# Optimization experiments

Measured on AMD Instinct MI355X. Metric: run time of the kernel, lower is better.

## Reference

```python
import jax, jax.numpy as jnp
import numpy as np

MODEL_DIM = 1024
NUM_HEADS = 16
HEAD_DIM = MODEL_DIM // NUM_HEADS


def setup_inputs() -> dict:
    key = jax.random.key(0)
    ks = jax.random.split(key, 5)
    B, T, D = 4, 2048, MODEL_DIM
    scale = 1.0 / np.sqrt(D)
    x = jax.random.normal(ks[0], (B, T, D), dtype=jnp.float32)
    W_qkv = jax.random.normal(ks[1], (D, 3 * D), dtype=jnp.float32) * scale
    b_qkv = jnp.zeros((3 * D,), dtype=jnp.float32)
    W_out = jax.random.normal(ks[2], (D, D), dtype=jnp.float32) * scale
    b_out = jnp.zeros((D,), dtype=jnp.float32)
    return {"x": x, "W_qkv": W_qkv, "b_qkv": b_qkv, "W_out": W_out, "b_out": b_out}


def reference(x, W_qkv, b_qkv, W_out, b_out):
    B, T, D = x.shape
    H, Hd = NUM_HEADS, HEAD_DIM
    qkv = x @ W_qkv + b_qkv                      # [B,T,3D]
    q, k, v = jnp.split(qkv, 3, axis=-1)
    # [B,T,D] -> [B,H,T,Hd]
    q = q.reshape(B, T, H, Hd).transpose(0, 2, 1, 3)
    k = k.reshape(B, T, H, Hd).transpose(0, 2, 1, 3)
    v = v.reshape(B, T, H, Hd).transpose(0, 2, 1, 3)
    scores = jnp.einsum('bhqd,bhkd->bhqk', q, k) * (1.0 / np.sqrt(Hd))
    causal = jnp.tril(jnp.ones((T, T), dtype=bool))
    scores = jnp.where(causal[None, None], scores, -jnp.inf)
    attn = jax.nn.softmax(scores, axis=-1)
    out = jnp.einsum('bhqk,bhkd->bhqd', attn, v)  # [B,H,T,Hd]
    out = out.transpose(0, 2, 1, 3).reshape(B, T, D)
    return out @ W_out + b_out
```

## Files before the change

### kernel.cpp

```cpp
#include <hip/hip_runtime.h>
#include <stdint.h>

#define T_SEQ   2048
#define DMODEL  1024
#define NHEADS  16
#define HDIM    64
#define BATCH   4
#define MROWS   (BATCH * T_SEQ)
#define QSCALE  0.18033688011112042f
#define DEFER_THR 6.0f

typedef __attribute__((ext_vector_type(4))) short bf16x4;
typedef __attribute__((ext_vector_type(8))) short bf16x8;
typedef __attribute__((ext_vector_type(4))) float f32x4;

__device__ __forceinline__ unsigned short f2b(float f) {
    union { float f; unsigned int i; } x;
    x.f = f;
    unsigned int r = x.i + 0x7FFFu + ((x.i >> 16) & 1u);
    return (unsigned short)(r >> 16);
}

__device__ __forceinline__ float fexp2(float x) {
#if __has_builtin(__builtin_amdgcn_exp2f)
    return __builtin_amdgcn_exp2f(x);
#else
    return __expf(x * 0.6931471805599453f);
#endif
}

__device__ __forceinline__ unsigned int pack2(float a, float b) {
#if __has_builtin(__builtin_amdgcn_cvt_pk_bf16_f32)
    auto r = __builtin_amdgcn_cvt_pk_bf16_f32(a, b);
    unsigned int u;
    __builtin_memcpy(&u, &r, 4);
    return u;
#else
    return ((unsigned int)f2b(a)) | (((unsigned int)f2b(b)) << 16);
#endif
}

__device__ __forceinline__ float max16(const f32x4 s[4]) {
    const float a = fmaxf(fmaxf(s[0][0], s[0][1]), fmaxf(s[0][2], s[0][3]));
    const float b = fmaxf(fmaxf(s[1][0], s[1][1]), fmaxf(s[1][2], s[1][3]));
    const float c = fmaxf(fmaxf(s[2][0], s[2][1]), fmaxf(s[2][2], s[2][3]));
    const float d = fmaxf(fmaxf(s[3][0], s[3][1]), fmaxf(s[3][2], s[3][3]));
    return fmaxf(fmaxf(a, b), fmaxf(c, d));
}

__device__ __forceinline__ void online_softmax(
    const f32x4 sg[4], float& m_, float& l_, f32x4 o_[4], bf16x4 pf_[4])
{
    float mc = max16(sg);
    mc = fmaxf(mc, __shfl_xor(mc, 16));
    mc = fmaxf(mc, __shfl_xor(mc, 32));
    if (__any(mc > m_ + DEFER_THR)) {
        const float mn    = fmaxf(m_, mc);
        const float alpha = fexp2(m_ - mn);
        l_ *= alpha;
        #pragma unroll
        for (int dt = 0; dt < 4; dt++)
            #pragma unroll
            for (int r = 0; r < 4; r++) o_[dt][r] *= alpha;
        m_ = mn;
    }
    float ps = 0.f;
    #pragma unroll
    for (int s = 0; s < 4; s++) {
        const float p0 = fexp2(sg[s][0] - m_);
        const float p1 = fexp2(sg[s][1] - m_);
        const float p2 = fexp2(sg[s][2] - m_);
        const float p3 = fexp2(sg[s][3] - m_);
        ps += (p0 + p1) + (p2 + p3);
        uint2 u;
        u.x = pack2(p0, p1);
        u.y = pack2(p2, p3);
        pf_[s] = *(bf16x4*)&u;
    }
    ps += __shfl_xor(ps, 16);
    ps += __shfl_xor(ps, 32);
    l_ += ps;
}

__device__ __forceinline__ void gl_lds16(const unsigned short* g, unsigned short* l) {
    __builtin_amdgcn_global_load_lds(
        (const __attribute__((address_space(1))) void*)g,
        (__attribute__((address_space(3))) void*)l,
        16, 0, 0);
}

__global__ __launch_bounds__(256) void cvt_bf16(
    const float* __restrict__ in, unsigned short* __restrict__ out, int n)
{
    const int i = (blockIdx.x * 256 + threadIdx.x) * 4;
    if (i + 3 < n) {
        const float4 v = *(const float4*)(in + i);
        ushort4 o;
        o.x = f2b(v.x); o.y = f2b(v.y); o.z = f2b(v.z); o.w = f2b(v.w);
        *(ushort4*)(out + i) = o;
    }
}

__global__ __launch_bounds__(256) void cvt_tr(
    const float* __restrict__ W, unsigned short* __restrict__ WT, int K, int N)
{
    __shared__ unsigned short s[32][33];
    const int n0 = blockIdx.x * 32, k0 = blockIdx.y * 32;
    const int tx = threadIdx.x & 31, ty = threadIdx.x >> 5;
    #pragma unroll
    for (int i = 0; i < 4; i++)
        s[ty + 8 * i][tx] = f2b(W[(size_t)(k0 + ty + 8 * i) * N + n0 + tx]);
    __syncthreads();
    #pragma unroll
    for (int i = 0; i < 4; i++)
        WT[(size_t)(n0 + ty + 8 * i) * K + k0 + tx] = s[tx][ty + 8 * i];
}

template<int KD, int NCOLS, int MODE>
__global__ __launch_bounds__(256) void gemm_mfma(
    const unsigned short* __restrict__ A,
    const unsigned short* __restrict__ BT,
    const float* __restrict__ bias,
    unsigned short* __restrict__ Oq,
    unsigned short* __restrict__ Ok,
    unsigned short* __restrict__ Ov,
    float* __restrict__ Of)
{
    __shared__ __align__(16) unsigned short aS[128 * 64];
    __shared__ __align__(16) unsigned short bS[128 * 64];

    const int tid  = threadIdx.x;
    const int lane = tid & 63;
    const int wave = tid >> 6;
    const int row  = lane & 15;
    const int quad = lane >> 4;
    const int wm   = wave >> 1;
    const int wn   = wave & 1;
    const int m0   = blockIdx.y * 128;
    const int n0   = blockIdx.x * 128;

    const int srow = lane >> 3;
    const int c8   = lane & 7;
    const int csw  = c8 ^ srow;

    const unsigned short* aG = A  + (size_t)(m0 + wave * 8 + srow) * KD + csw * 8;
    const unsigned short* bG = BT + (size_t)(n0 + wave * 8 + srow) * KD + csw * 8;

    f32x4 acc[4][4];
    const f32x4 z = {0.f, 0.f, 0.f, 0.f};
    #pragma unroll
    for (int i = 0; i < 4; i++)
        #pragma unroll
        for (int j = 0; j < 4; j++) acc[i][j] = z;

    for (int k0 = 0; k0 < KD; k0 += 64) {
        __syncthreads();
        #pragma unroll
        for (int c = 0; c < 4; c++) {
            gl_lds16(aG + c * (32 * KD), &aS[c * 2048 + wave * 512]);
            gl_lds16(bG + c * (32 * KD), &bS[c * 2048 + wave * 512]);
        }
        __syncthreads();
        aG += 64;
        bG += 64;

        #pragma unroll
        for (int ks = 0; ks < 2; ks++) {
            bf16x8 af[4], bf[4];
            const int cp = ((ks * 4 + quad) ^ (row & 7)) * 8;
            #pragma unroll
            for (int t = 0; t < 4; t++) {
                af[t] = *(const bf16x8*)(aS + (wm * 64 + t * 16 + row) * 64 + cp);
                bf[t] = *(const bf16x8*)(bS + (wn * 64 + t * 16 + row) * 64 + cp);
            }
            #pragma unroll
            for (int i = 0; i < 4; i++)
                #pragma unroll
                for (int j = 0; j < 4; j++)
                    acc[i][j] = __builtin_amdgcn_mfma_f32_16x16x32_bf16(af[i], bf[j], acc[i][j], 0, 0, 0);
        }
    }

    if (MODE == 0) {
        #pragma unroll
        for (int j = 0; j < 4; j++) {
            const int n  = n0 + wn * 64 + j * 16 + row;
            const float bi = bias[n];
            const int which = n >> 10;
            const int rem   = n & 1023;
            const int h     = rem >> 6;
            const int d     = rem & 63;
            #pragma unroll
            for (int i = 0; i < 4; i++) {
                const int mbase = m0 + wm * 64 + i * 16 + quad * 4;
                #pragma unroll
                for (int r = 0; r < 4; r++) {
                    const int m = mbase + r;
                    const int b = m >> 11;
                    const int t = m & 2047;
                    const int bh = b * NHEADS + h;
                    const float v = acc[i][j][r] + bi;
                    if (which == 0) {
                        Oq[((size_t)bh * T_SEQ + t) * HDIM + d] = f2b(v * QSCALE);
                    } else if (which == 1) {
                        Ok[((size_t)bh * T_SEQ + t) * HDIM + d] = f2b(v);
                    } else {
                        Ov[((size_t)bh * HDIM + d) * T_SEQ + t] = f2b(v);
                    }
                }
            }
        }
    } else {
        #pragma unroll
        for (int j = 0; j < 4; j++) {
            const int n  = n0 + wn * 64 + j * 16 + row;
            const float bi = bias[n];
            #pragma unroll
            for (int i = 0; i < 4; i++) {
                const int mbase = m0 + wm * 64 + i * 16 + quad * 4;
                #pragma unroll
                for (int r = 0; r < 4; r++)
                    Of[(size_t)(mbase + r) * NCOLS + n] = acc[i][j][r] + bi;
            }
        }
    }
}

__global__ __launch_bounds__(512, 4) void attn_mfma(
    const unsigned short* __restrict__ Q,
    const unsigned short* __restrict__ K,
    const unsigned short* __restrict__ VT,
    unsigned short* __restrict__ Out)
{
    __shared__ __align__(16) unsigned short kS[2][64 * 72];
    __shared__ __align__(16) unsigned short vS[2][64 * 72];

    const int tid  = threadIdx.x;
    const int lane = tid & 63;
    const int wave = tid >> 6;
    const int row  = lane & 15;
    const int quad = lane >> 4;

    const int bh = blockIdx.x;
    const int b  = bh >> 4;
    const int h  = bh & 15;
    const int P  = blockIdx.y;
    const int q0H = 128 * (15 - P) + 16 * wave;
    const int q0L = 128 * P        + 16 * wave;
    const int kend = 128 * (15 - P) + 128;

    const size_t qkbase = (size_t)bh * T_SEQ * HDIM;
    const size_t vtbase = (size_t)bh * HDIM * T_SEQ;

    const int krow0 = tid >> 3;
    const int c0    = tid & 7;
    const int lds0  = krow0 * 72 + c0 * 8;
    const int flat0 = tid * 8;

    const unsigned short* qpH = Q + qkbase + (size_t)(q0H + row) * HDIM + quad * 8;
    const bf16x8 qH0 = *(const bf16x8*)qpH;
    const bf16x8 qH1 = *(const bf16x8*)(qpH + 32);
    const unsigned short* qpL = Q + qkbase + (size_t)(q0L + row) * HDIM + quad * 8;
    const bf16x8 qL0 = *(const bf16x8*)qpL;
    const bf16x8 qL1 = *(const bf16x8*)(qpL + 32);

    const f32x4 z = {0.f, 0.f, 0.f, 0.f};
    f32x4 oH[4] = {z, z, z, z};
    f32x4 oL[4] = {z, z, z, z};
    float mH = -1e30f, lH = 0.f, mL = -1e30f, lL = 0.f;

    uint4 pk0 = *(const uint4*)(K  + qkbase + flat0);
    uint4 pv0 = *(const uint4*)(VT + vtbase + (size_t)krow0 * T_SEQ + c0 * 8);

    int buf = 0;
    for (int kb = 0; kb < kend; kb += 64) {
        *(uint4*)&kS[buf][lds0] = pk0;
        *(uint4*)&vS[buf][lds0] = pv0;
        __syncthreads();

        if (kb + 64 < kend) {
            const int kn = kb + 64;
            pk0 = *(const uint4*)(K  + qkbase + (size_t)kn * HDIM + flat0);
            pv0 = *(const uint4*)(VT + vtbase + (size_t)krow0 * T_SEQ + kn + c0 * 8);
        }

        const bool actH = (kb <= q0H);
        const bool actL = (kb <= q0L);

        bf16x4 pfH[4], pfL[4];

        if (actH) {
            f32x4 sH[4], sL[4];
            #pragma unroll
            for (int s = 0; s < 4; s++) {
                const int kbs = kb + s * 16;
                if (kbs <= q0H) {
                    const unsigned short* kp = &kS[buf][(s * 16 + row) * 72 + quad * 8];
                    const bf16x8 kf0 = *(const bf16x8*)kp;
                    const bf16x8 kf1 = *(const bf16x8*)(kp + 32);
                    f32x4 t = z;
                    t = __builtin_amdgcn_mfma_f32_16x16x32_bf16(kf0, qH0, t, 0, 0, 0);
                    t = __builtin_amdgcn_mfma_f32_16x16x32_bf16(kf1, qH1, t, 0, 0, 0);
                    if (kbs == q0H) {
                        #pragma unroll
                        for (int r = 0; r < 4; r++)
                            if (quad * 4 + r > row) t[r] = -1e30f;
                    }
                    sH[s] = t;
                    if (kbs <= q0L) {
                        f32x4 u = z;
                        u = __builtin_amdgcn_mfma_f32_16x16x32_bf16(kf0, qL0, u, 0, 0, 0);
                        u = __builtin_amdgcn_mfma_f32_16x16x32_bf16(kf1, qL1, u, 0, 0, 0);
                        if (kbs == q0L) {
                            #pragma unroll
                            for (int r = 0; r < 4; r++)
                                if (quad * 4 + r > row) u[r] = -1e30f;
                        }
                        sL[s] = u;
                    } else {
                        #pragma unroll
                        for (int r = 0; r < 4; r++) sL[s][r] = -1e30f;
                    }
                } else {
                    #pragma unroll
                    for (int r = 0; r < 4; r++) { sH[s][r] = -1e30f; sL[s][r] = -1e30f; }
                }
            }
            online_softmax(sH, mH, lH, oH, pfH);
            if (actL)
                online_softmax(sL, mL, lL, oL, pfL);

            #pragma unroll
            for (int s = 0; s < 4; s++) {
                const int kbs = kb + s * 16;
                if (kbs <= q0H) {
                    #pragma unroll
                    for (int dt = 0; dt < 4; dt++) {
                        const bf16x4 vf = *(const bf16x4*)&vS[buf][
                            (dt * 16 + row) * 72 + (s * 2 + (quad >> 1)) * 8 + (quad & 1) * 4];
                        oH[dt] = __builtin_amdgcn_mfma_f32_16x16x16bf16_1k(vf, pfH[s], oH[dt], 0, 0, 0);
                        if (kbs <= q0L)
                            oL[dt] = __builtin_amdgcn_mfma_f32_16x16x16bf16_1k(vf, pfL[s], oL[dt], 0, 0, 0);
                    }
                }
            }
        }

        buf ^= 1;
    }

    {
        const float rl = 1.f / lH;
        unsigned short* op = Out + ((size_t)(b * T_SEQ + q0H + row)) * DMODEL + h * HDIM + quad * 4;
        #pragma unroll
        for (int dt = 0; dt < 4; dt++) {
            uint2 u;
            u.x = pack2(oH[dt][0] * rl, oH[dt][1] * rl);
            u.y = pack2(oH[dt][2] * rl, oH[dt][3] * rl);
            *(uint2*)(op + dt * 16) = u;
        }
    }
    {
        const float rl = 1.f / lL;
        unsigned short* op = Out + ((size_t)(b * T_SEQ + q0L + row)) * DMODEL + h * HDIM + quad * 4;
        #pragma unroll
        for (int dt = 0; dt < 4; dt++) {
            uint2 u;
            u.x = pack2(oL[dt][0] * rl, oL[dt][1] * rl);
            u.y = pack2(oL[dt][2] * rl, oL[dt][3] * rl);
            *(uint2*)(op + dt * 16) = u;
        }
    }
}

extern "C" void kernel_launch(void* const* d_in, const int* in_sizes, int n_in,
                              void* d_out, int out_size, void* d_ws, size_t ws_size,
                              hipStream_t stream)
{
    const float* x    = (const float*)d_in[0];
    const float* Wqkv = (const float*)d_in[1];
    const float* bqkv = (const float*)d_in[2];
    const float* Wout = (const float*)d_in[3];
    const float* bout = (const float*)d_in[4];
    float* out = (float*)d_out;

    char* ws = (char*)d_ws;
    unsigned short* xb    = (unsigned short*)(ws + (size_t)0  * 1024 * 1024);
    unsigned short* WqkvT = (unsigned short*)(ws + (size_t)16 * 1024 * 1024);
    unsigned short* WoutT = (unsigned short*)(ws + (size_t)22 * 1024 * 1024);
    unsigned short* Qb    = (unsigned short*)(ws + (size_t)24 * 1024 * 1024);
    unsigned short* Kb    = (unsigned short*)(ws + (size_t)40 * 1024 * 1024);
    unsigned short* Vt    = (unsigned short*)(ws + (size_t)56 * 1024 * 1024);
    unsigned short* Ab    = (unsigned short*)(ws + (size_t)72 * 1024 * 1024);

    cvt_bf16<<<dim3(MROWS * DMODEL / 1024), 256, 0, stream>>>(x, xb, MROWS * DMODEL);
    cvt_tr<<<dim3(3 * DMODEL / 32, DMODEL / 32), 256, 0, stream>>>(Wqkv, WqkvT, DMODEL, 3 * DMODEL);
    cvt_tr<<<dim3(DMODEL / 32, DMODEL / 32), 256, 0, stream>>>(Wout, WoutT, DMODEL, DMODEL);

    gemm_mfma<DMODEL, 3 * DMODEL, 0><<<dim3(3 * DMODEL / 128, MROWS / 128), 256, 0, stream>>>(
        xb, WqkvT, bqkv, Qb, Kb, Vt, nullptr);

    attn_mfma<<<dim3(BATCH * NHEADS, 8), 512, 0, stream>>>(Qb, Kb, Vt, Ab);

    gemm_mfma<DMODEL, DMODEL, 1><<<dim3(DMODEL / 128, MROWS / 128), 256, 0, stream>>>(
        Ab, WoutT, bout, nullptr, nullptr, nullptr, out);
}
```

Baseline: 293.7 us.

## Add 256x256-tile 8-wave QKV GEMM with double-buffered direct-to-LDS loads

```diff
diff --git a/kernel.cpp b/kernel.cpp
--- a/kernel.cpp
+++ b/kernel.cpp
@@ -116,14 +116,190 @@
         WT[(size_t)(n0 + ty + 8 * i) * K + k0 + tx] = s[tx][ty + 8 * i];
 }
 
-template<int KD, int NCOLS, int MODE>
-__global__ __launch_bounds__(256) void gemm_mfma(
+__global__ __launch_bounds__(512, 2) void gemm_qkv8(
     const unsigned short* __restrict__ A,
     const unsigned short* __restrict__ BT,
     const float* __restrict__ bias,
     unsigned short* __restrict__ Oq,
     unsigned short* __restrict__ Ok,
-    unsigned short* __restrict__ Ov,
+    unsigned short* __restrict__ Ov)
+{
+    constexpr int KD = DMODEL;
+    constexpr int NK = KD / 64;
+    __shared__ __align__(16) unsigned short aS[2 * 256 * 64];
+    __shared__ __align__(16) unsigned short bS[2 * 256 * 64];
+
+    const int tid   = threadIdx.x;
+    const int lane  = tid & 63;
+    const int wave  = tid >> 6;
+    const int row16 = lane & 15;
+    const int quadL = lane >> 4;
+    const int wm    = wave >> 2;
+    const int wn    = wave & 3;
+    const int n0    = blockIdx.x * 256;
+    const int m0    = blockIdx.y * 256;
+
+    const int lrow = lane >> 3;
+    const int csw  = (lane & 7) ^ lrow;
+
+    const unsigned short* aB = A  + (size_t)(m0 + wave * 8 + lrow) * KD + csw * 8;
+    const unsigned short* bB = BT + (size_t)(n0 + wave * 8 + lrow) * KD + csw * 8;
+    unsigned short* aD = &aS[wave * 512];
+    unsigned short* bD = &bS[wave * 512];
+
+    const int sw0 = (quadL)     ^ (row16 & 7);
+    const int sw1 = (4 + quadL) ^ (row16 & 7);
+    const int aO  = (wm * 128 + row16) * 64;
+    const int bO  = (wn * 64  + row16) * 64;
+
+    f32x4 acc[8][4];
+    const f32x4 z = {0.f, 0.f, 0.f, 0.f};
+    #pragma unroll
+    for (int i = 0; i < 8; i++)
+        #pragma unroll
+        for (int j = 0; j < 4; j++) acc[i][j] = z;
+
+    gl_lds16(aB,                      aD);
+    gl_lds16(aB + (size_t)64  * KD,   aD + 64  * 64);
+    gl_lds16(aB + (size_t)128 * KD,   aD + 128 * 64);
+    gl_lds16(aB + (size_t)192 * KD,   aD + 192 * 64);
+    gl_lds16(bB,                      bD);
+    gl_lds16(bB + (size_t)64  * KD,   bD + 64  * 64);
+    gl_lds16(bB + (size_t)128 * KD,   bD + 128 * 64);
+    gl_lds16(bB + (size_t)192 * KD,   bD + 192 * 64);
+
+    for (int j = 0; j < NK; ++j) {
+        const int rb   = (j & 1) * 16384;
+        const int wb   = rb ^ 16384;
+        const int ksrc = (j + 1 < NK) ? (j + 1) * 64 : 0;
+        const unsigned short* aPk = aB + ksrc;
+        const unsigned short* bPk = bB + ksrc;
+
+        bf16x8 bfr[4][2];
+        bf16x8 a0, a1, a2, a3;
+
+        gl_lds16(aPk,                    aD + wb);
+        gl_lds16(aPk + (size_t)64 * KD,  aD + wb + 64 * 64);
+        asm volatile("s_waitcnt vmcnt(2)" ::: "memory");
+        __builtin_amdgcn_s_barrier();
+        #pragma unroll
+        for (int nf = 0; nf < 4; ++nf) {
+            bfr[nf][0] = *(const bf16x8*)&bS[rb + bO + nf * 1024 + sw0 * 8];
+            bfr[nf][1] = *(const bf16x8*)&bS[rb + bO + nf * 1024 + sw1 * 8];
+        }
+        a0 = *(const bf16x8*)&aS[rb + aO + 0 * 1024 + sw0 * 8];
+        a1 = *(const bf16x8*)&aS[rb + aO + 0 * 1024 + sw1 * 8];
+        a2 = *(const bf16x8*)&aS[rb + aO + 1 * 1024 + sw0 * 8];
+        a3 = *(const bf16x8*)&aS[rb + aO + 1 * 1024 + sw1 * 8];
+        asm volatile("s_waitcnt lgkmcnt(0)" ::: "memory");
+        __builtin_amdgcn_sched_barrier(0);
+        __builtin_amdgcn_s_setprio(1);
+        #pragma unroll
+        for (int nf = 0; nf < 4; ++nf) {
+            acc[0][nf] = __builtin_amdgcn_mfma_f32_16x16x32_bf16(a0, bfr[nf][0], acc[0][nf], 0, 0, 0);
+            acc[0][nf] = __builtin_amdgcn_mfma_f32_16x16x32_bf16(a1, bfr[nf][1], acc[0][nf], 0, 0, 0);
+            acc[1][nf] = __builtin_amdgcn_mfma_f32_16x16x32_bf16(a2, bfr[nf][0], acc[1][nf], 0, 0, 0);
+            acc[1][nf] = __builtin_amdgcn_mfma_f32_16x16x32_bf16(a3, bfr[nf][1], acc[1][nf], 0, 0, 0);
+        }
+        __builtin_amdgcn_s_setprio(0);
+        __builtin_amdgcn_s_barrier();
+
+        gl_lds16(aPk + (size_t)128 * KD, aD + wb + 128 * 64);
+        gl_lds16(aPk + (size_t)192 * KD, aD + wb + 192 * 64);
+        a0 = *(const bf16x8*)&aS[rb + aO + 2 * 1024 + sw0 * 8];
+        a1 = *(const bf16x8*)&aS[rb + aO + 2 * 1024 + sw1 * 8];
+        a2 = *(const bf16x8*)&aS[rb + aO + 3 * 1024 + sw0 * 8];
+        a3 = *(const bf16x8*)&aS[rb + aO + 3 * 1024 + sw1 * 8];
+        __builtin_amdgcn_s_barrier();
+        asm volatile("s_waitcnt lgkmcnt(0)" ::: "memory");
+        __builtin_amdgcn_sched_barrier(0);
+        __builtin_amdgcn_s_setprio(1);
+        #pragma unroll
+        for (int nf = 0; nf < 4; ++nf) {
+            acc[2][nf] = __builtin_amdgcn_mfma_f32_16x16x32_bf16(a0, bfr[nf][0], acc[2][nf], 0, 0, 0);
+            acc[2][nf] = __builtin_amdgcn_mfma_f32_16x16x32_bf16(a1, bfr[nf][1], acc[2][nf], 0, 0, 0);
+            acc[3][nf] = __builtin_amdgcn_mfma_f32_16x16x32_bf16(a2, bfr[nf][0], acc[3][nf], 0, 0, 0);
+            acc[3][nf] = __builtin_amdgcn_mfma_f32_16x16x32_bf16(a3, bfr[nf][1], acc[3][nf], 0, 0, 0);
+        }
+        __builtin_amdgcn_s_setprio(0);
+        __builtin_amdgcn_s_barrier();
+
+        gl_lds16(bPk,                    bD + wb);
+        gl_lds16(bPk + (size_t)64 * KD,  bD + wb + 64 * 64);
+        a0 = *(const bf16x8*)&aS[rb + aO + 4 * 1024 + sw0 * 8];
+        a1 = *(const bf16x8*)&aS[rb + aO + 4 * 1024 + sw1 * 8];
+        a2 = *(const bf16x8*)&aS[rb + aO + 5 * 1024 + sw0 * 8];
+        a3 = *(const bf16x8*)&aS[rb + aO + 5 * 1024 + sw1 * 8];
+        __builtin_amdgcn_s_barrier();
+        asm volatile("s_waitcnt lgkmcnt(0)" ::: "memory");
+        __builtin_amdgcn_sched_barrier(0);
+        __builtin_amdgcn_s_setprio(1);
+        #pragma unroll
+        for (int nf = 0; nf < 4; ++nf) {
+            acc[4][nf] = __builtin_amdgcn_mfma_f32_16x16x32_bf16(a0, bfr[nf][0], acc[4][nf], 0, 0, 0);
+            acc[4][nf] = __builtin_amdgcn_mfma_f32_16x16x32_bf16(a1, bfr[nf][1], acc[4][nf], 0, 0, 0);
+            acc[5][nf] = __builtin_amdgcn_mfma_f32_16x16x32_bf16(a2, bfr[nf][0], acc[5][nf], 0, 0, 0);
+            acc[5][nf] = __builtin_amdgcn_mfma_f32_16x16x32_bf16(a3, bfr[nf][1], acc[5][nf], 0, 0, 0);
+        }
+        __builtin_amdgcn_s_setprio(0);
+        __builtin_amdgcn_s_barrier();
+
+        gl_lds16(bPk + (size_t)128 * KD, bD + wb + 128 * 64);
+        gl_lds16(bPk + (size_t)192 * KD, bD + wb + 192 * 64);
+        a0 = *(const bf16x8*)&aS[rb + aO + 6 * 1024 + sw0 * 8];
+        a1 = *(const bf16x8*)&aS[rb + aO + 6 * 1024 + sw1 * 8];
+        a2 = *(const bf16x8*)&aS[rb + aO + 7 * 1024 + sw0 * 8];
+        a3 = *(const bf16x8*)&aS[rb + aO + 7 * 1024 + sw1 * 8];
+        __builtin_amdgcn_s_barrier();
+        asm volatile("s_waitcnt lgkmcnt(0)" ::: "memory");
+        __builtin_amdgcn_sched_barrier(0);
+        __builtin_amdgcn_s_setprio(1);
+        #pragma unroll
+        for (int nf = 0; nf < 4; ++nf) {
+            acc[6][nf] = __builtin_amdgcn_mfma_f32_16x16x32_bf16(a0, bfr[nf][0], acc[6][nf], 0, 0, 0);
+            acc[6][nf] = __builtin_amdgcn_mfma_f32_16x16x32_bf16(a1, bfr[nf][1], acc[6][nf], 0, 0, 0);
+            acc[7][nf] = __builtin_amdgcn_mfma_f32_16x16x32_bf16(a2, bfr[nf][0], acc[7][nf], 0, 0, 0);
+            acc[7][nf] = __builtin_amdgcn_mfma_f32_16x16x32_bf16(a3, bfr[nf][1], acc[7][nf], 0, 0, 0);
+        }
+        __builtin_amdgcn_s_setprio(0);
+        __builtin_amdgcn_s_barrier();
+    }
+
+    #pragma unroll
+    for (int nf = 0; nf < 4; ++nf) {
+        const int n  = n0 + wn * 64 + nf * 16 + row16;
+        const float bi = bias[n];
+        const int which = n >> 10;
+        const int rem   = n & 1023;
+        const int hh    = rem >> 6;
+        const int d     = rem & 63;
+        #pragma unroll
+        for (int mf = 0; mf < 8; ++mf) {
+            const int mbase = m0 + wm * 128 + mf * 16 + quadL * 4;
+            #pragma unroll
+            for (int r = 0; r < 4; ++r) {
+                const int mm = mbase + r;
+                const int bb = mm >> 11;
+                const int t  = mm & 2047;
+                const int bh = bb * NHEADS + hh;
+                const float v = acc[mf][nf][r] + bi;
+                if (which == 0) {
+                    Oq[((size_t)bh * T_SEQ + t) * HDIM + d] = f2b(v * QSCALE);
+                } else if (which == 1) {
+                    Ok[((size_t)bh * T_SEQ + t) * HDIM + d] = f2b(v);
+                } else {
+                    Ov[((size_t)bh * HDIM + d) * T_SEQ + t] = f2b(v);
+                }
+            }
+        }
+    }
+}
+
+template<int KD, int NCOLS>
+__global__ __launch_bounds__(256) void gemm_mfma(
+    const unsigned short* __restrict__ A,
+    const unsigned short* __restrict__ BT,
+    const float* __restrict__ bias,
     float* __restrict__ Of)
 {
     __shared__ __align__(16) unsigned short aS[128 * 64];
@@ -181,47 +357,16 @@
         }
     }
 
-    if (MODE == 0) {
-        #pragma unroll
-        for (int j = 0; j < 4; j++) {
-            const int n  = n0 + wn * 64 + j * 16 + row;
-            const float bi = bias[n];
-            const int which = n >> 10;
-            const int rem   = n & 1023;
-            const int h     = rem >> 6;
-            const int d     = rem & 63;
-            #pragma unroll
-            for (int i = 0; i < 4; i++) {
-                const int mbase = m0 + wm * 64 + i * 16 + quad * 4;
-                #pragma unroll
-                for (int r = 0; r < 4; r++) {
-                    const int m = mbase + r;
-                    const int b = m >> 11;
-                    const int t = m & 2047;
-                    const int bh = b * NHEADS + h;
-                    const float v = acc[i][j][r] + bi;
-                    if (which == 0) {
-                        Oq[((size_t)bh * T_SEQ + t) * HDIM + d] = f2b(v * QSCALE);
-                    } else if (which == 1) {
-                        Ok[((size_t)bh * T_SEQ + t) * HDIM + d] = f2b(v);
-                    } else {
-                        Ov[((size_t)bh * HDIM + d) * T_SEQ + t] = f2b(v);
-                    }
-                }
-            }
-        }
-    } else {
-        #pragma unroll
-        for (int j = 0; j < 4; j++) {
-            const int n  = n0 + wn * 64 + j * 16 + row;
-            const float bi = bias[n];
-            #pragma unroll
-            for (int i = 0; i < 4; i++) {
-                const int mbase = m0 + wm * 64 + i * 16 + quad * 4;
-                #pragma unroll
-                for (int r = 0; r < 4; r++)
-                    Of[(size_t)(mbase + r) * NCOLS + n] = acc[i][j][r] + bi;
-            }
+    #pragma unroll
+    for (int j = 0; j < 4; j++) {
+        const int n  = n0 + wn * 64 + j * 16 + row;
+        const float bi = bias[n];
+        #pragma unroll
+        for (int i = 0; i < 4; i++) {
+            const int mbase = m0 + wm * 64 + i * 16 + quad * 4;
+            #pragma unroll
+            for (int r = 0; r < 4; r++)
+                Of[(size_t)(mbase + r) * NCOLS + n] = acc[i][j][r] + bi;
         }
     }
 }
@@ -397,11 +542,11 @@
     cvt_tr<<<dim3(3 * DMODEL / 32, DMODEL / 32), 256, 0, stream>>>(Wqkv, WqkvT, DMODEL, 3 * DMODEL);
     cvt_tr<<<dim3(DMODEL / 32, DMODEL / 32), 256, 0, stream>>>(Wout, WoutT, DMODEL, DMODEL);
 
-    gemm_mfma<DMODEL, 3 * DMODEL, 0><<<dim3(3 * DMODEL / 128, MROWS / 128), 256, 0, stream>>>(
-        xb, WqkvT, bqkv, Qb, Kb, Vt, nullptr);
+    gemm_qkv8<<<dim3(3 * DMODEL / 256, MROWS / 256), 512, 0, stream>>>(
+        xb, WqkvT, bqkv, Qb, Kb, Vt);
 
     attn_mfma<<<dim3(BATCH * NHEADS, 8), 512, 0, stream>>>(Qb, Kb, Vt, Ab);
 
-    gemm_mfma<DMODEL, DMODEL, 1><<<dim3(DMODEL / 128, MROWS / 128), 256, 0, stream>>>(
-        Ab, WoutT, bout, nullptr, nullptr, nullptr, out);
-}
+    gemm_mfma<DMODEL, DMODEL><<<dim3(DMODEL / 128, MROWS / 128), 256, 0, stream>>>(
+        Ab, WoutT, bout, out);
+}
```

Result: slower. 315.1 us (+7.3%).

## Replace paired high/low query tiles with one query tile per attention block

Applied to the files above, without the earlier changes.

```diff
diff --git a/kernel.cpp b/kernel.cpp
--- a/kernel.cpp
+++ b/kernel.cpp
@@ -244,10 +244,9 @@
     const int bh = blockIdx.x;
     const int b  = bh >> 4;
     const int h  = bh & 15;
-    const int P  = blockIdx.y;
-    const int q0H = 128 * (15 - P) + 16 * wave;
-    const int q0L = 128 * P        + 16 * wave;
-    const int kend = 128 * (15 - P) + 128;
+    const int i  = 15 - (int)blockIdx.y;
+    const int q0 = 128 * i + 16 * wave;
+    const int kend = 128 * i + 128;
 
     const size_t qkbase = (size_t)bh * T_SEQ * HDIM;
     const size_t vtbase = (size_t)bh * HDIM * T_SEQ;
@@ -257,17 +256,13 @@
     const int lds0  = krow0 * 72 + c0 * 8;
     const int flat0 = tid * 8;
 
-    const unsigned short* qpH = Q + qkbase + (size_t)(q0H + row) * HDIM + quad * 8;
-    const bf16x8 qH0 = *(const bf16x8*)qpH;
-    const bf16x8 qH1 = *(const bf16x8*)(qpH + 32);
-    const unsigned short* qpL = Q + qkbase + (size_t)(q0L + row) * HDIM + quad * 8;
-    const bf16x8 qL0 = *(const bf16x8*)qpL;
-    const bf16x8 qL1 = *(const bf16x8*)(qpL + 32);
+    const unsigned short* qp = Q + qkbase + (size_t)(q0 + row) * HDIM + quad * 8;
+    const bf16x8 qf0 = *(const bf16x8*)qp;
+    const bf16x8 qf1 = *(const bf16x8*)(qp + 32);
 
     const f32x4 z = {0.f, 0.f, 0.f, 0.f};
-    f32x4 oH[4] = {z, z, z, z};
-    f32x4 oL[4] = {z, z, z, z};
-    float mH = -1e30f, lH = 0.f, mL = -1e30f, lL = 0.f;
+    f32x4 o[4] = {z, z, z, z};
+    float m_ = -1e30f, l_ = 0.f;
 
     uint4 pk0 = *(const uint4*)(K  + qkbase + flat0);
     uint4 pv0 = *(const uint4*)(VT + vtbase + (size_t)krow0 * T_SEQ + c0 * 8);
@@ -284,63 +279,43 @@
             pv0 = *(const uint4*)(VT + vtbase + (size_t)krow0 * T_SEQ + kn + c0 * 8);
         }
 
-        const bool actH = (kb <= q0H);
-        const bool actL = (kb <= q0L);
-
-        bf16x4 pfH[4], pfL[4];
-
-        if (actH) {
-            f32x4 sH[4], sL[4];
+        const bool act = (kb <= q0);
+
+        if (act) {
+            f32x4 sg[4];
+            bf16x4 pf[4];
             #pragma unroll
             for (int s = 0; s < 4; s++) {
                 const int kbs = kb + s * 16;
-                if (kbs <= q0H) {
+                if (kbs <= q0) {
                     const unsigned short* kp = &kS[buf][(s * 16 + row) * 72 + quad * 8];
                     const bf16x8 kf0 = *(const bf16x8*)kp;
                     const bf16x8 kf1 = *(const bf16x8*)(kp + 32);
                     f32x4 t = z;
-                    t = __builtin_amdgcn_mfma_f32_16x16x32_bf16(kf0, qH0, t, 0, 0, 0);
-                    t = __builtin_amdgcn_mfma_f32_16x16x32_bf16(kf1, qH1, t, 0, 0, 0);
-                    if (kbs == q0H) {
+                    t = __builtin_amdgcn_mfma_f32_16x16x32_bf16(kf0, qf0, t, 0, 0, 0);
+                    t = __builtin_amdgcn_mfma_f32_16x16x32_bf16(kf1, qf1, t, 0, 0, 0);
+                    if (kbs == q0) {
                         #pragma unroll
                         for (int r = 0; r < 4; r++)
                             if (quad * 4 + r > row) t[r] = -1e30f;
                     }
-                    sH[s] = t;
-                    if (kbs <= q0L) {
-                        f32x4 u = z;
-                        u = __builtin_amdgcn_mfma_f32_16x16x32_bf16(kf0, qL0, u, 0, 0, 0);
-                        u = __builtin_amdgcn_mfma_f32_16x16x32_bf16(kf1, qL1, u, 0, 0, 0);
-                        if (kbs == q0L) {
-                            #pragma unroll
-                            for (int r = 0; r < 4; r++)
-                                if (quad * 4 + r > row) u[r] = -1e30f;
-                        }
-                        sL[s] = u;
-                    } else {
-                        #pragma unroll
-                        for (int r = 0; r < 4; r++) sL[s][r] = -1e30f;
-                    }
+                    sg[s] = t;
                 } else {
                     #pragma unroll
-                    for (int r = 0; r < 4; r++) { sH[s][r] = -1e30f; sL[s][r] = -1e30f; }
+                    for (int r = 0; r < 4; r++) sg[s][r] = -1e30f;
                 }
             }
-            online_softmax(sH, mH, lH, oH, pfH);
-            if (actL)
-                online_softmax(sL, mL, lL, oL, pfL);
+            online_softmax(sg, m_, l_, o, pf);
 
             #pragma unroll
             for (int s = 0; s < 4; s++) {
                 const int kbs = kb + s * 16;
-                if (kbs <= q0H) {
+                if (kbs <= q0) {
                     #pragma unroll
                     for (int dt = 0; dt < 4; dt++) {
                         const bf16x4 vf = *(const bf16x4*)&vS[buf][
                             (dt * 16 + row) * 72 + (s * 2 + (quad >> 1)) * 8 + (quad & 1) * 4];
-                        oH[dt] = __builtin_amdgcn_mfma_f32_16x16x16bf16_1k(vf, pfH[s], oH[dt], 0, 0, 0);
-                        if (kbs <= q0L)
-                            oL[dt] = __builtin_amdgcn_mfma_f32_16x16x16bf16_1k(vf, pfL[s], oL[dt], 0, 0, 0);
+                        o[dt] = __builtin_amdgcn_mfma_f32_16x16x16bf16_1k(vf, pf[s], o[dt], 0, 0, 0);
                     }
                 }
             }
@@ -350,24 +325,13 @@
     }
 
     {
-        const float rl = 1.f / lH;
-        unsigned short* op = Out + ((size_t)(b * T_SEQ + q0H + row)) * DMODEL + h * HDIM + quad * 4;
+        const float rl = 1.f / l_;
+        unsigned short* op = Out + ((size_t)(b * T_SEQ + q0 + row)) * DMODEL + h * HDIM + quad * 4;
         #pragma unroll
         for (int dt = 0; dt < 4; dt++) {
             uint2 u;
-            u.x = pack2(oH[dt][0] * rl, oH[dt][1] * rl);
-            u.y = pack2(oH[dt][2] * rl, oH[dt][3] * rl);
-            *(uint2*)(op + dt * 16) = u;
-        }
-    }
-    {
-        const float rl = 1.f / lL;
-        unsigned short* op = Out + ((size_t)(b * T_SEQ + q0L + row)) * DMODEL + h * HDIM + quad * 4;
-        #pragma unroll
-        for (int dt = 0; dt < 4; dt++) {
-            uint2 u;
-            u.x = pack2(oL[dt][0] * rl, oL[dt][1] * rl);
-            u.y = pack2(oL[dt][2] * rl, oL[dt][3] * rl);
+            u.x = pack2(o[dt][0] * rl, o[dt][1] * rl);
+            u.y = pack2(o[dt][2] * rl, o[dt][3] * rl);
             *(uint2*)(op + dt * 16) = u;
         }
     }
@@ -400,7 +364,7 @@
     gemm_mfma<DMODEL, 3 * DMODEL, 0><<<dim3(3 * DMODEL / 128, MROWS / 128), 256, 0, stream>>>(
         xb, WqkvT, bqkv, Qb, Kb, Vt, nullptr);
 
-    attn_mfma<<<dim3(BATCH * NHEADS, 8), 512, 0, stream>>>(Qb, Kb, Vt, Ab);
+    attn_mfma<<<dim3(BATCH * NHEADS, 16), 512, 0, stream>>>(Qb, Kb, Vt, Ab);
 
     gemm_mfma<DMODEL, DMODEL, 1><<<dim3(DMODEL / 128, MROWS / 128), 256, 0, stream>>>(
         Ab, WoutT, bout, nullptr, nullptr, nullptr, out);
```

Measured after the change: 281.2 us. 4.3% less time.
